# Kernel tuning notes

Measured on AMD Instinct MI355X. Metric: run time of the kernel, lower is better.

Reference implementation:

```python
import jax, jax.numpy as jnp
import numpy as np

B, J, C = 4096, 17, 512       # batch, joints (length), channels (dim)
K, TOK, CH, H, KS, G = 3, 64, 1024, 8, 3, 8  # adj kernels, tokens_dim, channels_dim, heads, conv_large, gn groups
EPS = 1e-5


def setup_inputs() -> dict:
    key = jax.random.key(0)
    ks = jax.random.split(key, 16)
    r = lambda i, shp, s=0.02: jax.random.normal(ks[i], shp, jnp.float32) * s
    return {
        "x": jax.random.normal(ks[0], (B, J, C), jnp.float32),
        "adj": jax.random.uniform(ks[1], (K, J, J), jnp.float32) / J,
        "norm1_w": jnp.ones((J,), jnp.float32), "norm1_b": jnp.zeros((J,), jnp.float32),
        "gcn1_w": r(2, (K * C, C)), "gcn1_b": jnp.zeros((K * C,), jnp.float32),
        "dw_w": r(3, (C, 1, KS), 0.1), "dw_b": jnp.zeros((C,), jnp.float32),
        "gn1_w": jnp.ones((C,), jnp.float32), "gn1_b": jnp.zeros((C,), jnp.float32),
        "pw_w": r(4, (C, C)), "pw_b": jnp.zeros((C,), jnp.float32),
        "mlp1_w1": r(5, (TOK, J)), "mlp1_b1": jnp.zeros((TOK,), jnp.float32),
        "mlp1_w2": r(6, (J, TOK)), "mlp1_b2": jnp.zeros((J,), jnp.float32),
        "qkv_w": r(7, (3 * C, C)), "qkv_b": jnp.zeros((3 * C,), jnp.float32),
        "proj_w": r(8, (C, C)), "proj_b": jnp.zeros((C,), jnp.float32),
        "gnf_w": jnp.ones((C,), jnp.float32), "gnf_b": jnp.zeros((C,), jnp.float32),
        "norm2_w": jnp.ones((C,), jnp.float32), "norm2_b": jnp.zeros((C,), jnp.float32),
        "mlp2_w1": r(9, (CH, C)), "mlp2_b1": jnp.zeros((CH,), jnp.float32),
        "mlp2_w2": r(10, (C, CH)), "mlp2_b2": jnp.zeros((C,), jnp.float32),
        "gcn2_w": r(11, (K * C, C)), "gcn2_b": jnp.zeros((K * C,), jnp.float32),
    }


def _gelu(t):
    return jax.nn.gelu(t, approximate=False)  # torch nn.GELU default is exact erf


def _ln(t, w, b):  # LayerNorm over last axis
    m = t.mean(-1, keepdims=True)
    v = ((t - m) ** 2).mean(-1, keepdims=True)
    return (t - m) * jax.lax.rsqrt(v + EPS) * w + b


def _gn(t, w, b):  # GroupNorm(G, C) over (B, C, J)
    Bn, Cc, Jn = t.shape
    r = t.reshape(Bn, G, -1)
    m = r.mean(-1, keepdims=True)
    v = ((r - m) ** 2).mean(-1, keepdims=True)
    r = (r - m) * jax.lax.rsqrt(v + EPS)
    return r.reshape(Bn, Cc, Jn) * w[:, None] + b[:, None]


def _gcn(t, w, b, adj):  # t: (B,C,J); 1x1 conv to K*C then einsum with adj (K,J,J)
    y = jnp.einsum('bcj,oc->boj', t, w) + b[:, None]
    y = y.reshape(t.shape[0], K, C, t.shape[2])
    return jnp.einsum('bkcv,kvw->bcw', y, adj)


def reference(x, adj, norm1_w, norm1_b, gcn1_w, gcn1_b, dw_w, dw_b, gn1_w, gn1_b,
              pw_w, pw_b, mlp1_w1, mlp1_b1, mlp1_w2, mlp1_b2, qkv_w, qkv_b,
              proj_w, proj_b, gnf_w, gnf_b, norm2_w, norm2_b,
              mlp2_w1, mlp2_b1, mlp2_w2, mlp2_b2, gcn2_w, gcn2_b):
    res = x                                   # (B,J,C)
    xc = jnp.swapaxes(x, 1, 2)                # (B,C,J)
    xc = _ln(xc, norm1_w, norm1_b)            # LayerNorm over joints

    # --- branch 1: GCN ---
    x_gcn1 = _gcn(xc, gcn1_w, gcn1_b, adj)    # (B,C,J)

    # --- branch 2: depthwise conv + token MLP ---
    h = jax.lax.conv_general_dilated(xc, dw_w, (1,), [(KS // 2, KS // 2)],
                                     dimension_numbers=('NCH', 'OIH', 'NCH'),
                                     feature_group_count=C) + dw_b[:, None]
    h = _gelu(_gn(h, gn1_w, gn1_b))
    h = jnp.einsum('bcj,oc->boj', h, pw_w) + pw_b[:, None]      # 1x1 conv
    h = _gelu(jnp.einsum('bcj,tj->bct', h, mlp1_w1) + mlp1_b1)  # token mlp fc1
    h = jnp.einsum('bct,jt->bcj', h, mlp1_w2) + mlp1_b2         # token mlp fc2

    # --- branch 3: global spatial attention over joints ---
    dh = C // H
    qkv = jnp.einsum('bcj,oc->boj', xc, qkv_w) + qkv_b[:, None]  # (B,3C,J)
    q, k_, v_ = jnp.split(qkv, 3, axis=1)
    q = q.reshape(-1, H, dh, J); k_ = k_.reshape(-1, H, dh, J); v_ = v_.reshape(-1, H, dh, J)
    attn = jax.nn.softmax(jnp.einsum('bhdi,bhdj->bhij', q, k_) / jnp.sqrt(jnp.float32(dh)), axis=-1)
    sga = jnp.einsum('bhij,bhdj->bhdi', attn, v_).reshape(-1, C, J)
    sga = jnp.einsum('bcj,oc->boj', sga, proj_w) + proj_b[:, None]

    # --- fuse ---
    xc = _gelu(_gn(sga + x_gcn1 + h, gnf_w, gnf_b))
    xj = jnp.swapaxes(xc, 1, 2)               # (B,J,C)
    res_channel = xj
    xn = _ln(xj + res, norm2_w, norm2_b)      # LayerNorm over channels
    m = _gelu(jnp.einsum('bjc,hc->bjh', xn, mlp2_w1) + mlp2_b1)
    m = jnp.einsum('bjh,ch->bjc', m, mlp2_w2) + mlp2_b2
    g2 = _gcn(jnp.swapaxes(m, 1, 2), gcn2_w, gcn2_b, adj)  # (B,C,J)
    xj = res_channel + jnp.swapaxes(g2, 1, 2)
    return xj + res
```

## Files before the change

### kernel.cpp

```cpp
#include <hip/hip_runtime.h>
#include <stdint.h>

#define BB 4096
#define JJ 17
#define CC 512

typedef unsigned short u16;
typedef __bf16 bf16x8 __attribute__((ext_vector_type(8)));
typedef float  f32x4  __attribute__((ext_vector_type(4)));
typedef float  f32x2  __attribute__((ext_vector_type(2)));

__device__ __forceinline__ float bf2f(u16 u){ return __uint_as_float(((uint32_t)u)<<16); }
__device__ __forceinline__ u16 f2bf(float f){
  uint32_t u = __float_as_uint(f);
  u += 0x7fffu + ((u>>16)&1u);
  return (u16)(u>>16);
}
__device__ __forceinline__ void unpk2(uint32_t u, float& lo, float& hi){
  lo = __uint_as_float(u<<16);
  hi = __uint_as_float(u & 0xffff0000u);
}
__device__ __forceinline__ float gelu_f(float x){
  float x2 = x*x;
  float y2 = x*fmaf(0.0713548162726f, x2, 1.59576912161f);
  float ey = __builtin_amdgcn_exp2f(y2*1.44269504089f);
  return fmaf(-x, __builtin_amdgcn_rcpf(ey+1.f), x);
}
__device__ __forceinline__ void gll16(const void* g, void* l){
  __builtin_amdgcn_global_load_lds(
      (const __attribute__((address_space(1))) void*)g,
      (__attribute__((address_space(3))) void*)l, 16, 0, 0);
}

__global__ void k_cvt7(const float* __restrict__ s0,const float* __restrict__ s1,
                       const float* __restrict__ s2,const float* __restrict__ s3,
                       const float* __restrict__ s4,const float* __restrict__ s5,
                       const float* __restrict__ s6, u16* __restrict__ out){
  int i = blockIdx.x*blockDim.x + threadIdx.x;
  if (i >= 3932160) return;
  const float* src; int off;
  if      (i < 786432)  { src=s0; off=0; }
  else if (i < 1572864) { src=s1; off=786432; }
  else if (i < 1835008) { src=s2; off=1572864; }
  else if (i < 2097152) { src=s3; off=1835008; }
  else if (i < 2621440) { src=s4; off=2097152; }
  else if (i < 3145728) { src=s5; off=2621440; }
  else                  { src=s6; off=3145728; }
  out[i] = f2bf(src[i-off]);
}

__global__ void k_tokprep(const float* __restrict__ w1, const float* __restrict__ w2,
                          float* __restrict__ w1p, float* __restrict__ w2p){
  int i = blockIdx.x*blockDim.x + threadIdx.x;
  if (i >= 1280) return;
  int t = i/20, j = i%20;
  w1p[i] = (j<17) ? w1[t*17+j] : 0.f;
  w2p[i] = (j<17) ? w2[j*64+t] : 0.f;
}

__global__ __launch_bounds__(512) void k_pre(
    const float* __restrict__ x, int b0,
    const float* __restrict__ n1w, const float* __restrict__ n1b,
    const float* __restrict__ dww, const float* __restrict__ dwb,
    const float* __restrict__ gn1w, const float* __restrict__ gn1b,
    u16* __restrict__ xc, u16* __restrict__ hgn)
{
  int b = blockIdx.x, c = threadIdx.x;
  const float* xp = x + (size_t)(b0+b)*JJ*CC + c;
  float v[JJ]; float s = 0.f;
  #pragma unroll
  for (int j=0;j<JJ;j++){ v[j] = xp[(size_t)j*CC]; s += v[j]; }
  float mn = s*(1.f/JJ); float var = 0.f;
  #pragma unroll
  for (int j=0;j<JJ;j++){ float d=v[j]-mn; var += d*d; }
  float rr = rsqrtf(var*(1.f/JJ)+1e-5f);
  float xcv[JJ];
  #pragma unroll
  for (int j=0;j<JJ;j++) xcv[j] = (v[j]-mn)*rr*n1w[j] + n1b[j];
  u16* xo = xc + (size_t)b*JJ*CC + c;
  #pragma unroll
  for (int j=0;j<JJ;j++) xo[(size_t)j*CC] = f2bf(xcv[j]);
  float w0=dww[c*3+0], w1=dww[c*3+1], w2=dww[c*3+2], db=dwb[c];
  float h[JJ];
  #pragma unroll
  for (int j=0;j<JJ;j++){
    float a = db + w1*xcv[j];
    if (j>0)    a += w0*xcv[j-1];
    if (j<JJ-1) a += w2*xcv[j+1];
    h[j] = a;
  }
  float ss=0.f, sq=0.f;
  #pragma unroll
  for (int j=0;j<JJ;j++){ ss += h[j]; sq += h[j]*h[j]; }
  for (int off=32; off; off>>=1){ ss += __shfl_xor(ss,off); sq += __shfl_xor(sq,off); }
  float gm = ss*(1.f/(64.f*JJ));
  float gr = rsqrtf(sq*(1.f/(64.f*JJ)) - gm*gm + 1e-5f);
  float gw = gn1w[c], gb = gn1b[c];
  u16* ho = hgn + (size_t)b*JJ*CC + c;
  #pragma unroll
  for (int j=0;j<JJ;j++){
    float t = (h[j]-gm)*gr*gw + gb;
    ho[(size_t)j*CC] = f2bf(gelu_f(t));
  }
}

template<int DO_GELU, int DO_ADD>
__global__ __launch_bounds__(512,4) void gemm_r5(
    const u16* __restrict__ A, const u16* __restrict__ W, const float* __restrict__ bias,
    u16* __restrict__ out, const u16* __restrict__ add0, const u16* __restrict__ add1,
    int M, int N, int K, int NXT)
{
  __shared__ __align__(16) u16 lds[36864];
  const int tid = threadIdx.x;
  const int wid = tid>>6, lane = tid&63;

  const int nwg = gridDim.x;
  const int q8 = nwg>>3, r8 = nwg&7;
  const int xcd = blockIdx.x & 7, sub = blockIdx.x >> 3;
  const int wg = (xcd<r8 ? xcd*(q8+1) : r8*(q8+1)+(xcd-r8)*q8) + sub;
  const int n0 = (wg % NXT)*256;
  const int m0 = (wg / NXT)*128;

  const int wm = wid>>2, wn = wid&3;
  const int lr = lane&15, lg = lane>>4;
  const int T  = K>>5;

  const int agsw = ((tid&3) ^ ((tid>>3)&3))<<3;
  const u16* gA  = A + (size_t)(m0 + (tid>>2))*K + agsw;
  const u16* gB0 = W + (size_t)(n0 + (tid>>2))*K + agsw;
  const u16* gB1 = W + (size_t)(n0 + 128 + (tid>>2))*K + agsw;
  const int dstl = tid*8;

  const int g8 = (lg ^ ((lr>>1)&3))<<3;
  const int offA0 = (wm*64+lr)*32 + g8;
  const int offB0 = 4096 + (wn*64+lr)*32 + g8;

  f32x4 acc[4][4];
  #pragma unroll
  for (int i=0;i<4;i++)
    #pragma unroll
    for (int j=0;j<4;j++) acc[i][j] = (f32x4){0.f,0.f,0.f,0.f};

  auto STAGE = [&](int t, int sofs){
    gll16(gA  + t*32, lds + sofs + dstl);
    gll16(gB0 + t*32, lds + sofs + 4096 + dstl);
    gll16(gB1 + t*32, lds + sofs + 8192 + dstl);
  };

  STAGE(0, 0); STAGE(1, 12288);
  asm volatile("s_waitcnt vmcnt(3)" ::: "memory");
  __builtin_amdgcn_s_barrier();

  int s0 = 0, s1 = 12288, s2 = 24576;
  for (int t=0; t<T; ++t){
    const bool more = (t+2 < T);
    if (more) STAGE(t+2, s2);
    bf16x8 av[4], bv[4];
    #pragma unroll
    for (int i=0;i<4;i++) av[i] = *(const bf16x8*)&lds[s0 + offA0 + i*512];
    #pragma unroll
    for (int j=0;j<4;j++) bv[j] = *(const bf16x8*)&lds[s0 + offB0 + j*512];
    asm volatile("s_waitcnt lgkmcnt(0)" ::: "memory");
    __builtin_amdgcn_sched_barrier(0);
    __builtin_amdgcn_s_setprio(1);
    #pragma unroll
    for (int i=0;i<4;i++)
      #pragma unroll
      for (int j=0;j<4;j++)
        acc[i][j] = __builtin_amdgcn_mfma_f32_16x16x32_bf16(av[i], bv[j], acc[i][j], 0,0,0);
    __builtin_amdgcn_s_setprio(0);
    if (more) asm volatile("s_waitcnt vmcnt(3)" ::: "memory");
    else      asm volatile("s_waitcnt vmcnt(0)" ::: "memory");
    __builtin_amdgcn_s_barrier();
    const int tmp = s0; s0 = s1; s1 = s2; s2 = tmp;
  }

  const int rbase = lg*4;
  #pragma unroll
  for (int i=0;i<4;i++){
    #pragma unroll
    for (int j=0;j<4;j++){
      const int col  = n0 + wn*64 + j*16 + lr;
      const int row0 = m0 + wm*64 + i*16 + rbase;
      const float bvl = bias[col];
      #pragma unroll
      for (int r=0;r<4;r++){
        size_t idx = (size_t)(row0+r)*N + col;
        float v = acc[i][j][r] + bvl;
        if (DO_ADD)  v += bf2f(add0[idx]) + bf2f(add1[idx]);
        if (DO_GELU) v = gelu_f(v);
        out[idx] = f2bf(v);
      }
    }
  }
}

template<int FINAL>
__global__ __launch_bounds__(512) void k_gcn2(
    const u16* __restrict__ G, const float* __restrict__ adj,
    u16* __restrict__ xg,
    const u16* __restrict__ rc, const float* __restrict__ x, int b0,
    float* __restrict__ out)
{
  __shared__ __align__(16) float adjp[51*20];
  const int tid = threadIdx.x;
  for (int i=tid; i<1020; i+=512){
    int r=i/20, cl=i%20;
    adjp[i] = (cl<17) ? adj[r*17+cl] : 0.f;
  }
  __syncthreads();

  const int sl  = tid>>7;
  const int l   = tid&127;
  const int c0  = l*4;
  const int bl  = blockIdx.x*4 + sl;

  float acc[JJ][4];
  #pragma unroll
  for (int w=0;w<JJ;w++)
    #pragma unroll
    for (int e=0;e<4;e++) acc[w][e]=0.f;

  const u16* gbase = G + (size_t)bl*JJ*1536 + c0;
  #pragma unroll 3
  for (int kv=0; kv<51; kv++){
    const int k = kv/JJ, v = kv - k*JJ;
    uint2 yu = *(const uint2*)(gbase + (size_t)v*1536 + k*512);
    float y0,y1,y2,y3;
    unpk2(yu.x, y0, y1);
    unpk2(yu.y, y2, y3);
    const f32x4* arow = (const f32x4*)&adjp[kv*20];
    f32x4 a0=arow[0], a1=arow[1], a2=arow[2], a3=arow[3];
    float a16 = adjp[kv*20+16];
    float ar[JJ] = {a0[0],a0[1],a0[2],a0[3], a1[0],a1[1],a1[2],a1[3],
                    a2[0],a2[1],a2[2],a2[3], a3[0],a3[1],a3[2],a3[3], a16};
    #pragma unroll
    for (int w=0;w<JJ;w++){
      acc[w][0] += y0*ar[w];
      acc[w][1] += y1*ar[w];
      acc[w][2] += y2*ar[w];
      acc[w][3] += y3*ar[w];
    }
  }

  if (FINAL==0){
    u16* xo = xg + (size_t)bl*JJ*CC + c0;
    #pragma unroll
    for (int w=0;w<JJ;w++){
      uint2 o;
      o.x = (uint32_t)f2bf(acc[w][0]) | ((uint32_t)f2bf(acc[w][1])<<16);
      o.y = (uint32_t)f2bf(acc[w][2]) | ((uint32_t)f2bf(acc[w][3])<<16);
      *(uint2*)(xo + (size_t)w*CC) = o;
    }
  } else {
    const size_t gb = (size_t)(b0+bl)*JJ*CC + c0;
    const u16* rp = rc + (size_t)bl*JJ*CC + c0;
    #pragma unroll
    for (int w=0;w<JJ;w++){
      uint2 ru = *(const uint2*)(rp + (size_t)w*CC);
      float r0,r1,r2,r3;
      unpk2(ru.x, r0, r1);
      unpk2(ru.y, r2, r3);
      f32x4 xv = *(const f32x4*)(x + gb + (size_t)w*CC);
      f32x4 o;
      o[0]=acc[w][0]+r0+xv[0]; o[1]=acc[w][1]+r1+xv[1];
      o[2]=acc[w][2]+r2+xv[2]; o[3]=acc[w][3]+r3+xv[3];
      *(f32x4*)(out + gb + (size_t)w*CC) = o;
    }
  }
}

__global__ __launch_bounds__(512) void k_attn(const u16* __restrict__ Gqkv, u16* __restrict__ sga){
  __shared__ __align__(16) u16 qs[8*17*72];
  __shared__ __align__(16) u16 ks_[8*17*72];
  __shared__ __align__(16) float at[8*17*20];
  int b = blockIdx.x, tid = threadIdx.x;
  int h = tid>>6, d = tid&63;
  const u16* base = Gqkv + (size_t)b*JJ*1536;
  float vv[JJ];
  #pragma unroll
  for (int i=0;i<JJ;i++){
    qs [(h*JJ+i)*72 + d] = base[(size_t)i*1536 +        h*64 + d];
    ks_[(h*JJ+i)*72 + d] = base[(size_t)i*1536 +  512 + h*64 + d];
    vv[i] = bf2f(base[(size_t)i*1536 + 1024 + h*64 + d]);
  }
  __syncthreads();
  for (int p=d; p<289; p+=64){
    int i=p/JJ, j=p-i*JJ;
    const u16* qrow = &qs [(h*JJ+i)*72];
    const u16* krow = &ks_[(h*JJ+j)*72];
    float a=0.f;
    #pragma unroll
    for (int t=0;t<8;t++){
      bf16x8 q8 = *(const bf16x8*)&qrow[t*8];
      bf16x8 k8 = *(const bf16x8*)&krow[t*8];
      #pragma unroll
      for (int e=0;e<8;e++) a += (float)q8[e]*(float)k8[e];
    }
    at[(h*JJ+i)*20 + j] = a*0.125f;
  }
  __syncthreads();
  if (d < JJ){
    float* row = &at[(h*JJ+d)*20];
    f32x4 r0=((f32x4*)row)[0], r1=((f32x4*)row)[1], r2=((f32x4*)row)[2], r3=((f32x4*)row)[3];
    float e16=row[16];
    float rv[JJ]={r0[0],r0[1],r0[2],r0[3],r1[0],r1[1],r1[2],r1[3],
                  r2[0],r2[1],r2[2],r2[3],r3[0],r3[1],r3[2],r3[3],e16};
    float mx=-1e30f;
    #pragma unroll
    for (int j=0;j<JJ;j++) mx=fmaxf(mx,rv[j]);
    float sm=0.f;
    #pragma unroll
    for (int j=0;j<JJ;j++){ rv[j]=__builtin_amdgcn_exp2f((rv[j]-mx)*1.44269504089f); sm+=rv[j]; }
    float inv=1.f/sm;
    #pragma unroll
    for (int j=0;j<JJ;j++) row[j]=rv[j]*inv;
  }
  __syncthreads();
  #pragma unroll
  for (int i=0;i<JJ;i++){
    const float* row = &at[(h*JJ+i)*20];
    f32x4 r0=((const f32x4*)row)[0], r1=((const f32x4*)row)[1],
          r2=((const f32x4*)row)[2], r3=((const f32x4*)row)[3];
    float a = r0[0]*vv[0]+r0[1]*vv[1]+r0[2]*vv[2]+r0[3]*vv[3]
            + r1[0]*vv[4]+r1[1]*vv[5]+r1[2]*vv[6]+r1[3]*vv[7]
            + r2[0]*vv[8]+r2[1]*vv[9]+r2[2]*vv[10]+r2[3]*vv[11]
            + r3[0]*vv[12]+r3[1]*vv[13]+r3[2]*vv[14]+r3[3]*vv[15]
            + row[16]*vv[16];
    sga[((size_t)b*JJ+i)*CC + h*64 + d] = f2bf(a);
  }
}

__global__ __launch_bounds__(512) void k_tok(const u16* __restrict__ Hpw,
    const float* __restrict__ w1p, const float* __restrict__ w2p,
    const float* __restrict__ b1, const float* __restrict__ b2,
    u16* __restrict__ h2o){
  __shared__ __align__(16) float w1s[1280], w2s[1280];
  __shared__ __align__(8) float b1s[64];
  __shared__ __align__(8) float b2s[20];
  const int tid = threadIdx.x;
  for (int i=tid; i<1280; i+=512){ w1s[i]=w1p[i]; w2s[i]=w2p[i]; }
  if (tid<64) b1s[tid]=b1[tid];
  if (tid<20) b2s[tid] = (tid<17) ? b2[tid] : 0.f;
  __syncthreads();

  const int bl = blockIdx.x*2 + (tid>>8);
  const int c0 = tid&255;
  const u16* hp = Hpw + (size_t)bl*JJ*CC;
  f32x2 h0p[9], h1p[9];
  #pragma unroll
  for (int p=0;p<8;p++){
    h0p[p] = (f32x2){bf2f(hp[(size_t)(2*p)*CC + c0]),     bf2f(hp[(size_t)(2*p+1)*CC + c0])};
    h1p[p] = (f32x2){bf2f(hp[(size_t)(2*p)*CC + c0+256]), bf2f(hp[(size_t)(2*p+1)*CC + c0+256])};
  }
  h0p[8] = (f32x2){bf2f(hp[(size_t)16*CC + c0]),     0.f};
  h1p[8] = (f32x2){bf2f(hp[(size_t)16*CC + c0+256]), 0.f};

  f32x2 a20[9], a21[9];
  #pragma unroll
  for (int p=0;p<9;p++){
    f32x2 bb = *(const f32x2*)&b2s[2*p];
    a20[p]=bb; a21[p]=bb;
  }

  #pragma unroll 2
  for (int t=0;t<64;t++){
    const f32x2* w1v = (const f32x2*)&w1s[t*20];
    f32x2 s0 = (f32x2){b1s[t], 0.f};
    f32x2 s1 = s0;
    #pragma unroll
    for (int p=0;p<9;p++){
      s0 = __builtin_elementwise_fma(h0p[p], w1v[p], s0);
      s1 = __builtin_elementwise_fma(h1p[p], w1v[p], s1);
    }
    float a0 = gelu_f(s0[0] + s0[1]);
    float a1 = gelu_f(s1[0] + s1[1]);
    const f32x2* w2v = (const f32x2*)&w2s[t*20];
    f32x2 a0b = (f32x2){a0,a0};
    f32x2 a1b = (f32x2){a1,a1};
    #pragma unroll
    for (int p=0;p<9;p++){
      a20[p] = __builtin_elementwise_fma(a0b, w2v[p], a20[p]);
      a21[p] = __builtin_elementwise_fma(a1b, w2v[p], a21[p]);
    }
  }
  u16* ho = h2o + (size_t)bl*JJ*CC;
  #pragma unroll
  for (int j=0;j<JJ;j++){
    ho[(size_t)j*CC + c0]       = f2bf(a20[j>>1][j&1]);
    ho[(size_t)j*CC + c0 + 256] = f2bf(a21[j>>1][j&1]);
  }
}

__global__ __launch_bounds__(512) void k_fuse(const u16* __restrict__ s,
    const float* __restrict__ x, int b0,
    const float* __restrict__ gfw, const float* __restrict__ gfb,
    const float* __restrict__ n2w, const float* __restrict__ n2b,
    u16* __restrict__ rc, u16* __restrict__ xn){
  __shared__ float rS[8][JJ], rQ[8][JJ];
  int b = blockIdx.x, c = threadIdx.x;
  int wave = c>>6, lane = c&63;
  const u16* sp = s + (size_t)b*JJ*CC + c;
  float sv[JJ];
  #pragma unroll
  for (int j=0;j<JJ;j++) sv[j]=bf2f(sp[(size_t)j*CC]);
  float ss=0.f, sq=0.f;
  #pragma unroll
  for (int j=0;j<JJ;j++){ ss+=sv[j]; sq+=sv[j]*sv[j]; }
  for (int off=32; off; off>>=1){ ss += __shfl_xor(ss,off); sq += __shfl_xor(sq,off); }
  float gm = ss*(1.f/1088.f);
  float gr = rsqrtf(sq*(1.f/1088.f) - gm*gm + 1e-5f);
  float gw=gfw[c], gb=gfb[c];
  const float* xp = x + (size_t)(b0+b)*JJ*CC + c;
  u16* rp = rc + (size_t)b*JJ*CC + c;
  float t[JJ];
  #pragma unroll
  for (int j=0;j<JJ;j++){
    float v = gelu_f((sv[j]-gm)*gr*gw + gb);
    rp[(size_t)j*CC] = f2bf(v);
    t[j] = v + xp[(size_t)j*CC];
  }
  #pragma unroll
  for (int j=0;j<JJ;j++){
    float a=t[j], q=a*a;
    for (int off=32; off; off>>=1){ a+=__shfl_xor(a,off); q+=__shfl_xor(q,off); }
    if (lane==0){ rS[wave][j]=a; rQ[wave][j]=q; }
  }
  __syncthreads();
  float wN=n2w[c], bN=n2b[c];
  u16* xo = xn + (size_t)b*JJ*CC + c;
  #pragma unroll
  for (int j=0;j<JJ;j++){
    float S=0.f,Q=0.f;
    #pragma unroll
    for (int w=0;w<8;w++){ S+=rS[w][j]; Q+=rQ[w][j]; }
    float mn=S*(1.f/512.f);
    float r2=rsqrtf(Q*(1.f/512.f)-mn*mn+1e-5f);
    xo[(size_t)j*CC]=f2bf((t[j]-mn)*r2*wN+bN);
  }
}

extern "C" void kernel_launch(void* const* d_in, const int* in_sizes, int n_in,
                              void* d_out, int out_size, void* d_ws, size_t ws_size,
                              hipStream_t stream)
{
  const float* x      = (const float*)d_in[0];
  const float* adj    = (const float*)d_in[1];
  const float* n1w    = (const float*)d_in[2];
  const float* n1b    = (const float*)d_in[3];
  const float* gcn1_w = (const float*)d_in[4];
  const float* gcn1_b = (const float*)d_in[5];
  const float* dw_w   = (const float*)d_in[6];
  const float* dw_b   = (const float*)d_in[7];
  const float* gn1_w  = (const float*)d_in[8];
  const float* gn1_b  = (const float*)d_in[9];
  const float* pw_w   = (const float*)d_in[10];
  const float* pw_b   = (const float*)d_in[11];
  const float* m1w1   = (const float*)d_in[12];
  const float* m1b1   = (const float*)d_in[13];
  const float* m1w2   = (const float*)d_in[14];
  const float* m1b2   = (const float*)d_in[15];
  const float* qkv_w  = (const float*)d_in[16];
  const float* qkv_b  = (const float*)d_in[17];
  const float* proj_w = (const float*)d_in[18];
  const float* proj_b = (const float*)d_in[19];
  const float* gnf_w  = (const float*)d_in[20];
  const float* gnf_b  = (const float*)d_in[21];
  const float* n2w    = (const float*)d_in[22];
  const float* n2b    = (const float*)d_in[23];
  const float* m2w1   = (const float*)d_in[24];
  const float* m2b1   = (const float*)d_in[25];
  const float* m2w2   = (const float*)d_in[26];
  const float* m2b2   = (const float*)d_in[27];
  const float* gcn2_w = (const float*)d_in[28];
  const float* gcn2_b = (const float*)d_in[29];
  float* out = (float*)d_out;

  char* ws = (char*)d_ws;
  const size_t WBYTES = (size_t)3932160*2;
  const size_t TPBYTES = 2560*4;

  const int cands[5] = {4096,2048,1024,512,256};
  int NB = 0;
  for (int ci=0; ci<5; ci++){
    size_t need = WBYTES + TPBYTES + (size_t)cands[ci]*JJ*2*(1536 + 4*512);
    if (need <= ws_size){ NB = cands[ci]; break; }
  }
  if (NB == 0) return;

  u16* wb = (u16*)ws;
  float* w1p = (float*)(ws + WBYTES);
  float* w2p = w1p + 1280;
  char* p = ws + WBYTES + TPBYTES;
  const size_t SZ_BIGc = (size_t)NB*JJ*1536*2;
  const size_t SZTc    = (size_t)NB*JJ*512*2;
  u16* big = (u16*)p;               p += SZ_BIGc;
  u16* t0  = (u16*)p;               p += SZTc;
  u16* t1  = (u16*)p;               p += SZTc;
  u16* t2  = (u16*)p;               p += SZTc;
  u16* t3  = (u16*)p;

  u16 *wg1=wb, *wqkv=wb+786432, *wpw=wb+1572864, *wproj=wb+1835008,
      *wm1=wb+2097152, *wm2=wb+2621440, *wg2=wb+3145728;

  k_cvt7<<<(3932160+255)/256,256,0,stream>>>(gcn1_w,qkv_w,pw_w,proj_w,m2w1,m2w2,gcn2_w,wb);
  k_tokprep<<<5,256,0,stream>>>(m1w1,m1w2,w1p,w2p);

  const int M2 = NB*JJ;
  const int MT = M2/128;
  for (int b0 = 0; b0 < BB; b0 += NB){
    k_pre<<<NB,512,0,stream>>>(x,b0,n1w,n1b,dw_w,dw_b,gn1_w,gn1_b, t0, t1);
    gemm_r5<0,0><<<MT*6,512,0,stream>>>(t0,wg1,gcn1_b,big,nullptr,nullptr,M2,1536,512,6);
    k_gcn2<0><<<NB/4,512,0,stream>>>(big,adj,t2,nullptr,nullptr,0,nullptr);
    gemm_r5<0,0><<<MT*6,512,0,stream>>>(t0,wqkv,qkv_b,big,nullptr,nullptr,M2,1536,512,6);
    k_attn<<<NB,512,0,stream>>>(big,t3);
    gemm_r5<0,0><<<MT*2,512,0,stream>>>(t1,wpw,pw_b,t0,nullptr,nullptr,M2,512,512,2);
    k_tok<<<NB/2,512,0,stream>>>(t0,w1p,w2p,m1b1,m1b2,t1);
    gemm_r5<0,1><<<MT*2,512,0,stream>>>(t3,wproj,proj_b,t0,t2,t1,M2,512,512,2);
    k_fuse<<<NB,512,0,stream>>>(t0,x,b0,gnf_w,gnf_b,n2w,n2b,t1,t2);
    gemm_r5<1,0><<<MT*4,512,0,stream>>>(t2,wm1,m2b1,big,nullptr,nullptr,M2,1024,512,4);
    gemm_r5<0,0><<<MT*2,512,0,stream>>>(big,wm2,m2b2,t0,nullptr,nullptr,M2,512,1024,2);
    gemm_r5<0,0><<<MT*6,512,0,stream>>>(t0,wg2,gcn2_b,big,nullptr,nullptr,M2,1536,512,6);
    k_gcn2<1><<<NB/4,512,0,stream>>>(big,adj,nullptr,t1,x,b0,out);
  }
}
```

Baseline: 1.358 ms.

## Rewrite token MLP kernel to use bf16 MFMA with LDS-staged transposed inputs

```diff
diff --git a/kernel.cpp b/kernel.cpp
--- a/kernel.cpp
+++ b/kernel.cpp
@@ -8,7 +8,6 @@
 typedef unsigned short u16;
 typedef __bf16 bf16x8 __attribute__((ext_vector_type(8)));
 typedef float  f32x4  __attribute__((ext_vector_type(4)));
-typedef float  f32x2  __attribute__((ext_vector_type(2)));
 
 __device__ __forceinline__ float bf2f(u16 u){ return __uint_as_float(((uint32_t)u)<<16); }
 __device__ __forceinline__ u16 f2bf(float f){
@@ -50,12 +49,11 @@
 }
 
 __global__ void k_tokprep(const float* __restrict__ w1, const float* __restrict__ w2,
-                          float* __restrict__ w1p, float* __restrict__ w2p){
+                          u16* __restrict__ w1m, u16* __restrict__ w2m){
   int i = blockIdx.x*blockDim.x + threadIdx.x;
-  if (i >= 1280) return;
-  int t = i/20, j = i%20;
-  w1p[i] = (j<17) ? w1[t*17+j] : 0.f;
-  w2p[i] = (j<17) ? w2[j*64+t] : 0.f;
+  if (i < 2560){ int t=i/40, j=i%40; w1m[i] = (j<17) ? f2bf(w1[t*17+j]) : (u16)0; }
+  int k = i - 2560;
+  if (k >= 0 && k < 2304){ int j=k/72, t=k%72; w2m[k] = (j<17 && t<64) ? f2bf(w2[j*64+t]) : (u16)0; }
 }
 
 __global__ __launch_bounds__(512) void k_pre(
@@ -331,64 +329,95 @@
   }
 }
 
-__global__ __launch_bounds__(512) void k_tok(const u16* __restrict__ Hpw,
-    const float* __restrict__ w1p, const float* __restrict__ w2p,
+__global__ __launch_bounds__(256) void k_tok(const u16* __restrict__ Hpw,
+    const u16* __restrict__ w1m, const u16* __restrict__ w2m,
     const float* __restrict__ b1, const float* __restrict__ b2,
     u16* __restrict__ h2o){
-  __shared__ __align__(16) float w1s[1280], w2s[1280];
-  __shared__ __align__(8) float b1s[64];
-  __shared__ __align__(8) float b2s[20];
-  const int tid = threadIdx.x;
-  for (int i=tid; i<1280; i+=512){ w1s[i]=w1p[i]; w2s[i]=w2p[i]; }
-  if (tid<64) b1s[tid]=b1[tid];
-  if (tid<20) b2s[tid] = (tid<17) ? b2[tid] : 0.f;
+  __shared__ __align__(16) u16 lds[31488];
+  __shared__ float b1s[64], b2s[32];
+  const int tid = threadIdx.x, wid = tid>>6, lane = tid&63;
+  const int lr = lane&15, lg = lane>>4;
+  const int bl = blockIdx.x;
+  const f32x4 zz = {0.f,0.f,0.f,0.f};
+
+  for (int i=tid; i<2560; i+=256) lds[26624+i] = w1m[i];
+  for (int i=tid; i<2304; i+=256) lds[29184+i] = w2m[i];
+  if (tid<64) b1s[tid] = b1[tid];
+  if (tid<32) b2s[tid] = (tid<17) ? b2[tid] : 0.f;
+  {
+    const int base = tid*40;
+    lds[base+17]=0; lds[base+18]=0; lds[base+19]=0;
+    #pragma unroll
+    for (int q=0;q<5;q++) *(uint2*)&lds[base+20+q*4] = (uint2){0u,0u};
+  }
   __syncthreads();
 
-  const int bl = blockIdx.x*2 + (tid>>8);
-  const int c0 = tid&255;
   const u16* hp = Hpw + (size_t)bl*JJ*CC;
-  f32x2 h0p[9], h1p[9];
-  #pragma unroll
-  for (int p=0;p<8;p++){
-    h0p[p] = (f32x2){bf2f(hp[(size_t)(2*p)*CC + c0]),     bf2f(hp[(size_t)(2*p+1)*CC + c0])};
-    h1p[p] = (f32x2){bf2f(hp[(size_t)(2*p)*CC + c0+256]), bf2f(hp[(size_t)(2*p+1)*CC + c0+256])};
-  }
-  h0p[8] = (f32x2){bf2f(hp[(size_t)16*CC + c0]),     0.f};
-  h1p[8] = (f32x2){bf2f(hp[(size_t)16*CC + c0+256]), 0.f};
-
-  f32x2 a20[9], a21[9];
-  #pragma unroll
-  for (int p=0;p<9;p++){
-    f32x2 bb = *(const f32x2*)&b2s[2*p];
-    a20[p]=bb; a21[p]=bb;
-  }
-
-  #pragma unroll 2
-  for (int t=0;t<64;t++){
-    const f32x2* w1v = (const f32x2*)&w1s[t*20];
-    f32x2 s0 = (f32x2){b1s[t], 0.f};
-    f32x2 s1 = s0;
-    #pragma unroll
-    for (int p=0;p<9;p++){
-      s0 = __builtin_elementwise_fma(h0p[p], w1v[p], s0);
-      s1 = __builtin_elementwise_fma(h1p[p], w1v[p], s1);
-    }
-    float a0 = gelu_f(s0[0] + s0[1]);
-    float a1 = gelu_f(s1[0] + s1[1]);
-    const f32x2* w2v = (const f32x2*)&w2s[t*20];
-    f32x2 a0b = (f32x2){a0,a0};
-    f32x2 a1b = (f32x2){a1,a1};
-    #pragma unroll
-    for (int p=0;p<9;p++){
-      a20[p] = __builtin_elementwise_fma(a0b, w2v[p], a20[p]);
-      a21[p] = __builtin_elementwise_fma(a1b, w2v[p], a21[p]);
-    }
-  }
-  u16* ho = h2o + (size_t)bl*JJ*CC;
-  #pragma unroll
-  for (int j=0;j<JJ;j++){
-    ho[(size_t)j*CC + c0]       = f2bf(a20[j>>1][j&1]);
-    ho[(size_t)j*CC + c0 + 256] = f2bf(a21[j>>1][j&1]);
+  u16* op = h2o + (size_t)bl*JJ*CC;
+
+  for (int pass=0; pass<2; ++pass){
+    const int cbase = pass*256;
+    for (int idx=tid; idx<1088; idx+=256){
+      int j = idx>>6, cq = (idx&63)<<2;
+      uint2 u = *(const uint2*)(hp + (size_t)j*CC + cbase + cq);
+      lds[(cq  )*40 + j] = (u16)(u.x & 0xffffu);
+      lds[(cq+1)*40 + j] = (u16)(u.x >> 16);
+      lds[(cq+2)*40 + j] = (u16)(u.y & 0xffffu);
+      lds[(cq+3)*40 + j] = (u16)(u.y >> 16);
+    }
+    __syncthreads();
+
+    bf16x8 av1[4];
+    #pragma unroll
+    for (int mt=0;mt<4;mt++) av1[mt] = *(const bf16x8*)&lds[26624 + (mt*16+lr)*40 + lg*8];
+    #pragma unroll
+    for (int nt=0;nt<4;nt++){
+      const int cl = wid*64 + nt*16 + lr;
+      bf16x8 bv = *(const bf16x8*)&lds[cl*40 + lg*8];
+      #pragma unroll
+      for (int mt=0;mt<4;mt++){
+        f32x4 ac = __builtin_amdgcn_mfma_f32_16x16x32_bf16(av1[mt], bv, zz, 0,0,0);
+        const int t0 = mt*16 + lg*4;
+        float g0 = gelu_f(ac[0] + b1s[t0+0]);
+        float g1 = gelu_f(ac[1] + b1s[t0+1]);
+        float g2 = gelu_f(ac[2] + b1s[t0+2]);
+        float g3 = gelu_f(ac[3] + b1s[t0+3]);
+        uint2 pk;
+        pk.x = (uint32_t)f2bf(g0) | ((uint32_t)f2bf(g1)<<16);
+        pk.y = (uint32_t)f2bf(g2) | ((uint32_t)f2bf(g3)<<16);
+        const int gi = (10240 + cl*64 + t0) ^ ((cl&7)<<3);
+        *(uint2*)&lds[gi] = pk;
+      }
+    }
+    asm volatile("s_waitcnt lgkmcnt(0)" ::: "memory");
+    __builtin_amdgcn_sched_barrier(0);
+
+    bf16x8 av2[2][2];
+    #pragma unroll
+    for (int mt=0;mt<2;mt++)
+      #pragma unroll
+      for (int kt=0;kt<2;kt++)
+        av2[mt][kt] = *(const bf16x8*)&lds[29184 + (mt*16+lr)*72 + kt*32 + lg*8];
+    #pragma unroll
+    for (int nt=0;nt<4;nt++){
+      const int cl = wid*64 + nt*16 + lr;
+      f32x4 a20 = zz, a21 = zz;
+      #pragma unroll
+      for (int kt=0;kt<2;kt++){
+        const int gi = (10240 + cl*64 + kt*32 + lg*8) ^ ((cl&7)<<3);
+        bf16x8 bv2 = *(const bf16x8*)&lds[gi];
+        a20 = __builtin_amdgcn_mfma_f32_16x16x32_bf16(av2[0][kt], bv2, a20, 0,0,0);
+        a21 = __builtin_amdgcn_mfma_f32_16x16x32_bf16(av2[1][kt], bv2, a21, 0,0,0);
+      }
+      const int c = cbase + cl;
+      #pragma unroll
+      for (int r=0;r<4;r++){
+        const int j = lg*4 + r;
+        op[(size_t)j*CC + c] = f2bf(a20[r] + b2s[j]);
+      }
+      if (lg==0) op[(size_t)16*CC + c] = f2bf(a21[0] + b2s[16]);
+    }
+    __syncthreads();
   }
 }
 
@@ -478,7 +507,7 @@
 
   char* ws = (char*)d_ws;
   const size_t WBYTES = (size_t)3932160*2;
-  const size_t TPBYTES = 2560*4;
+  const size_t TPBYTES = (2560+2304)*2;
 
   const int cands[5] = {4096,2048,1024,512,256};
   int NB = 0;
@@ -489,8 +518,8 @@
   if (NB == 0) return;
 
   u16* wb = (u16*)ws;
-  float* w1p = (float*)(ws + WBYTES);
-  float* w2p = w1p + 1280;
+  u16* w1m = (u16*)(ws + WBYTES);
+  u16* w2m = w1m + 2560;
   char* p = ws + WBYTES + TPBYTES;
   const size_t SZ_BIGc = (size_t)NB*JJ*1536*2;
   const size_t SZTc    = (size_t)NB*JJ*512*2;
@@ -504,7 +533,7 @@
       *wm1=wb+2097152, *wm2=wb+2621440, *wg2=wb+3145728;
 
   k_cvt7<<<(3932160+255)/256,256,0,stream>>>(gcn1_w,qkv_w,pw_w,proj_w,m2w1,m2w2,gcn2_w,wb);
-  k_tokprep<<<5,256,0,stream>>>(m1w1,m1w2,w1p,w2p);
+  k_tokprep<<<19,256,0,stream>>>(m1w1,m1w2,w1m,w2m);
 
   const int M2 = NB*JJ;
   const int MT = M2/128;
@@ -515,7 +544,7 @@
     gemm_r5<0,0><<<MT*6,512,0,stream>>>(t0,wqkv,qkv_b,big,nullptr,nullptr,M2,1536,512,6);
     k_attn<<<NB,512,0,stream>>>(big,t3);
     gemm_r5<0,0><<<MT*2,512,0,stream>>>(t1,wpw,pw_b,t0,nullptr,nullptr,M2,512,512,2);
-    k_tok<<<NB/2,512,0,stream>>>(t0,w1p,w2p,m1b1,m1b2,t1);
+    k_tok<<<NB,256,0,stream>>>(t0,w1m,w2m,m1b1,m1b2,t1);
     gemm_r5<0,1><<<MT*2,512,0,stream>>>(t3,wproj,proj_b,t0,t2,t1,M2,512,512,2);
     k_fuse<<<NB,512,0,stream>>>(t0,x,b0,gnf_w,gnf_b,n2w,n2b,t1,t2);
     gemm_r5<1,0><<<MT*4,512,0,stream>>>(t2,wm1,m2b1,big,nullptr,nullptr,M2,1024,512,4);
```

New measurement: 1.328 ms. 1.02x faster.
